# Kernel optimization log

Measured on AMD Instinct MI355X. Metric: run time of the kernel, lower is better.

## Reference

```python
import jax, jax.numpy as jnp
import numpy as np

B, L, D = 4, 2048, 64
N_HEAD = 4
LOCALITY = 0.2
PI = 3.141592653589793


def setup_inputs() -> dict:
    key = jax.random.key(0)
    k1, k2, k3 = jax.random.split(key, 3)
    mesh = jax.random.uniform(k1, (B, L, 2), dtype=jnp.float32)
    inputs = jax.random.normal(k2, (B, L, D), dtype=jnp.float32)
    lmda = jax.random.uniform(k3, (N_HEAD, 1, 1), dtype=jnp.float32)
    return {"mesh": mesh, "inputs": inputs, "lmda": lmda}


def reference(mesh, inputs, lmda):
    FMAX = jnp.finfo(jnp.float32).max
    # pairwise squared distances: (B, L, L)
    diff = mesh[:, :, None, :] - mesh[:, None, :, :]
    m_dist = jnp.sum(diff * diff, axis=-1)
    # per-head scale in (0, inf): tan(pi/4 * (1-eps) * (1 + sin(lmda)))
    scale = jnp.tan(0.25 * PI * (1.0 - 1e-07) * (1.0 + jnp.sin(lmda)))  # (H,1,1)
    scaled = m_dist[:, None, :, :] * scale  # (B, H, L, L)
    # row-wise quantile threshold (linear interpolation, matching torch.quantile)
    thresh = jnp.quantile(scaled, LOCALITY, axis=-1, keepdims=True)  # (B,H,L,1)
    masked = jnp.where(scaled <= thresh, scaled, FMAX)
    att = jax.nn.softmax(-masked, axis=-1)  # (B, H, L, L)
    # aggregate: (B,H,L,L) x (B,L,D) -> (B,L,H,D) -> (B,L,H*D)
    conv = jnp.einsum('bhnj,bjd->bnhd', att, inputs)
    conv = conv.reshape(inputs.shape[0], -1, N_HEAD * inputs.shape[-1])
    return jnp.concatenate([inputs, conv], axis=-1)
```

## Files before the change

### kernel.cpp

```cpp
#include <hip/hip_runtime.h>
#include <math.h>

#ifndef M_PI
#define M_PI 3.14159265358979323846
#endif

namespace {
constexpr int B_ = 4;
constexpr int L_ = 2048;
constexpr int D_ = 64;
constexpr int H_ = 4;
constexpr int RB = 8;
constexpr int KT = 64;
constexpr int NTILE = L_ / KT;
constexpr int CAPC = 256;
constexpr int OUTW = D_ + H_ * D_;
constexpr int APS = 2064;
constexpr int ABYTES = 2 * APS;
constexpr int BBYTES = KT * D_ * 2;
constexpr int BUFB = ABYTES + BBYTES;
}

typedef __attribute__((ext_vector_type(8))) short bf16x8;
typedef __attribute__((ext_vector_type(4))) float f32x4;

__device__ __forceinline__ unsigned bf16_rne(float x) {
    unsigned u = __float_as_uint(x);
    return (u + 0x7fffu + ((u >> 16) & 1u)) >> 16;
}

__device__ __forceinline__ unsigned cvt_pk_bf16(float lo, float hi) {
    unsigned r;
    asm("v_cvt_pk_bf16_f32 %0, %1, %2" : "=v"(r) : "v"(lo), "v"(hi));
    return r;
}

#if defined(__has_builtin)
#if __has_builtin(__builtin_amdgcn_exp2f)
#define EXP2F(x) __builtin_amdgcn_exp2f(x)
#endif
#endif
#ifndef EXP2F
#define EXP2F(x) __expf((x) * 0.69314718055994531f)
#endif

#define LDS_FENCE() __builtin_amdgcn_s_waitcnt(0xC07F)

__global__ __launch_bounds__(256) void prep_kernel(const float* __restrict__ inputs,
                                                   char* __restrict__ ws) {
    const int blk = blockIdx.x;
    const int b = blk >> 6;
    const int r6 = blk & 63;
    const int tile = r6 >> 2;
    const int qr = r6 & 3;
    const int t = threadIdx.x;
    const float* inb = inputs + ((size_t)b * L_ + tile * 128) * D_;
    char* wsb = ws + (size_t)b * (L_ * D_ * 2) + tile * (128 * D_ * 2);
    #pragma unroll
    for (int i = 0; i < 4; ++i) {
        const int idx = qr * 1024 + i * 256 + t;
        const int n  = idx & 63;
        const int kp = idx >> 6;
        const int kl = kp << 1;
        const float x0 = inb[kl * D_ + n];
        const float x1 = inb[(kl + 1) * D_ + n];
        const unsigned a = bf16_rne(x0);
        const unsigned c = bf16_rne(x1);
        const int chunk = (kl >> 3) * 64 + n;
        const int e = kl & 7;
        *reinterpret_cast<unsigned*>(wsb + chunk * 16 + e * 2) = a | (c << 16);
    }
}

__global__ __launch_bounds__(512, 8) void posatt_kernel(
    const float* __restrict__ mesh,
    const float* __restrict__ inputs,
    const float* __restrict__ lmda,
    const char* __restrict__ ws,
    float* __restrict__ out)
{
    __shared__ __align__(16) char s_u1[2 * BUFB];
    __shared__ float s_scale[H_];
    __shared__ float s_thD[RB];
    __shared__ float s_d409[RB], s_d410[RB];
    __shared__ float s_wsum[RB][H_];
    __shared__ unsigned s_ccw[8];

    const int t = threadIdx.x;
    const int l = t & 63;
    const int w = t >> 6;
    const int blk = blockIdx.x;
    const int b = blk >> 8;
    const int n0 = (blk & 255) * RB;

    const float2* meshg = reinterpret_cast<const float2*>(mesh) + (size_t)b * L_;

    if (t < H_) {
        const double lam = (double)lmda[t];
        const float C = (float)(0.25 * M_PI * (1.0 - 1e-07));
        const float s1 = (float)sin(lam);
        const float arg = __fmul_rn(C, __fadd_rn(1.0f, s1));
        s_scale[t] = (float)tan((double)arg);
    }
    if (t < RB) { s_d409[t] = 0.0f; s_d410[t] = 0.0f; }
    __syncthreads();

    {
        unsigned* hw = reinterpret_cast<unsigned*>(s_u1) + w * 256;
        float* cw = reinterpret_cast<float*>(s_u1 + 8192) + w * CAPC;
        const int rl = w;
        const float2 me = meshg[n0 + rl];
        *reinterpret_cast<uint4*>(&hw[l * 4]) = make_uint4(0u, 0u, 0u, 0u);
        if (l == 0) s_ccw[w] = 0u;
        LDS_FENCE();
        #pragma unroll 4
        for (int it = 0; it < 32; ++it) {
            const int j = (it << 6) + l;
            const float2 mj = meshg[j];
            const float dx = __fsub_rn(me.x, mj.x);
            const float dy = __fsub_rn(me.y, mj.y);
            const float d = __fadd_rn(__fmul_rn(dx, dx), __fmul_rn(dy, dy));
            int bin = (int)(d * 128.0f); bin = bin < 255 ? bin : 255;
            atomicAdd(&hw[bin], 1u);
        }
        LDS_FENCE();
        int lo, hi; unsigned base;
        {
            const uint4 hv = *reinterpret_cast<const uint4*>(&hw[l * 4]);
            const unsigned p0 = hv.x, p1 = p0 + hv.y, p2 = p1 + hv.z, p3 = p2 + hv.w;
            unsigned sc = p3;
            #pragma unroll
            for (int off = 1; off < 64; off <<= 1) {
                const unsigned uu = __shfl_up(sc, off);
                if (l >= off) sc += uu;
            }
            const unsigned eb = sc - p3;
            const unsigned cum[4] = {eb + p0, eb + p1, eb + p2, eb + p3};
            int flo = -1, fhi = -1; unsigned fbase = 0u;
            #pragma unroll
            for (int e = 0; e < 4; ++e) {
                const unsigned prev = e ? cum[e - 1] : eb;
                if (cum[e] > 409u && prev <= 409u) { flo = l * 4 + e; fbase = prev; }
                if (cum[e] > 410u && prev <= 410u) { fhi = l * 4 + e; }
            }
            const unsigned long long bmlo = __ballot(flo >= 0);
            const int srclo = (int)__builtin_ctzll(bmlo);
            lo = __shfl(flo, srclo);
            base = __shfl(fbase, srclo);
            const unsigned long long bmhi = __ballot(fhi >= 0);
            hi = __shfl(fhi, (int)__builtin_ctzll(bmhi));
        }
        #pragma unroll 4
        for (int it = 0; it < 32; ++it) {
            const int j = (it << 6) + l;
            const float2 mj = meshg[j];
            const float dx = __fsub_rn(me.x, mj.x);
            const float dy = __fsub_rn(me.y, mj.y);
            const float d = __fadd_rn(__fmul_rn(dx, dx), __fmul_rn(dy, dy));
            int bin = (int)(d * 128.0f); bin = bin < 255 ? bin : 255;
            if (bin >= lo && bin <= hi) {
                const unsigned p = atomicAdd(&s_ccw[w], 1u);
                if (p < (unsigned)CAPC) cw[p] = d;
            }
        }
        LDS_FENCE();
        const int m = (int)min(s_ccw[w], (unsigned)CAPC);
        const unsigned k409 = 409u - base;
        const unsigned k410 = 410u - base;
        const float lo_edge = (float)lo * 0.0078125f;
        const float sc2 = 32768.0f / (float)(hi - lo + 1);
        *reinterpret_cast<uint4*>(&hw[l * 4]) = make_uint4(0u, 0u, 0u, 0u);
        LDS_FENCE();
        #pragma unroll 2
        for (int ci = l; ci < m; ci += 64) {
            const float v = cw[ci];
            int b2 = (int)(__fmul_rn(__fsub_rn(v, lo_edge), sc2));
            b2 = b2 < 255 ? b2 : 255; b2 = b2 > 0 ? b2 : 0;
            atomicAdd(&hw[b2], 1u);
        }
        LDS_FENCE();
        int lo2, hi2; unsigned base2;
        {
            const uint4 hv = *reinterpret_cast<const uint4*>(&hw[l * 4]);
            const unsigned p0 = hv.x, p1 = p0 + hv.y, p2 = p1 + hv.z, p3 = p2 + hv.w;
            unsigned sc = p3;
            #pragma unroll
            for (int off = 1; off < 64; off <<= 1) {
                const unsigned uu = __shfl_up(sc, off);
                if (l >= off) sc += uu;
            }
            const unsigned eb = sc - p3;
            const unsigned cum[4] = {eb + p0, eb + p1, eb + p2, eb + p3};
            int flo = -1, fhi = -1; unsigned fbase = 0u;
            #pragma unroll
            for (int e = 0; e < 4; ++e) {
                const unsigned prev = e ? cum[e - 1] : eb;
                if (cum[e] > k409 && prev <= k409) { flo = l * 4 + e; fbase = prev; }
                if (cum[e] > k410 && prev <= k410) { fhi = l * 4 + e; }
            }
            const unsigned long long bmlo = __ballot(flo >= 0);
            const int srclo = (int)__builtin_ctzll(bmlo);
            lo2 = __shfl(flo, srclo);
            base2 = __shfl(fbase, srclo);
            const unsigned long long bmhi = __ballot(fhi >= 0);
            hi2 = __shfl(fhi, (int)__builtin_ctzll(bmhi));
        }
        if (l == 0) s_ccw[w] = 0u;
        LDS_FENCE();
        float* c2 = reinterpret_cast<float*>(hw);
        #pragma unroll 2
        for (int ci = l; ci < m; ci += 64) {
            const float v = cw[ci];
            int b2 = (int)(__fmul_rn(__fsub_rn(v, lo_edge), sc2));
            b2 = b2 < 255 ? b2 : 255; b2 = b2 > 0 ? b2 : 0;
            if (b2 >= lo2 && b2 <= hi2) {
                const unsigned p = atomicAdd(&s_ccw[w], 1u);
                if (p < 256u) c2[p] = v;
            }
        }
        LDS_FENCE();
        const int c = (int)min(s_ccw[w], 256u);
        const int q409 = (int)(k409 - base2);
        const int q410 = (int)(k410 - base2);
        #pragma unroll 1
        for (int cc0 = 0; cc0 < c; cc0 += 64) {
            const int ci = cc0 + l;
            const float v = (ci < c) ? c2[ci] : 0.0f;
            int lt = 0, le = 0;
            #pragma unroll 4
            for (int i = 0; i < c; ++i) {
                const float u = c2[i];
                lt += (u < v) ? 1 : 0;
                le += (u <= v) ? 1 : 0;
            }
            if (ci < c) {
                if (lt <= q409 && q409 < le) s_d409[rl] = v;
                if (lt <= q410 && q410 < le) s_d410[rl] = v;
            }
        }
    }
    __syncthreads();

    if (t < RB) {
        const float pos = 0.2f * 2047.0f;
        const float g = pos - 409.0f;
        const float lw = 1.0f - g;
        s_thD[t] = __fadd_rn(__fmul_rn(s_d409[t], lw), __fmul_rn(s_d410[t], g));
    }
    __syncthreads();

    const int jp = t & 31;
    const int rr = (t >> 5) & 7;
    const int h2 = t >> 8;
    const float2 me_b = meshg[n0 + rr];
    const float thD = s_thD[rr];
    constexpr float LOG2E = 1.4426950408889634f;
    const float cA = __fmul_rn(-LOG2E, s_scale[h2]);
    const float cB = __fmul_rn(-LOG2E, s_scale[h2 + 2]);
    const int row16 = h2 * 8 + rr;
    const int ks4q_w = jp >> 2;
    const int chunk_w = ks4q_w * 16 + row16;
    const int chunkSw_w = chunk_w ^ (ks4q_w & 7);
    const int aoff0 = (chunkSw_w << 4) + ((jp & 3) << 2);
    float waccA = 0.0f, waccB = 0.0f;

    const int p_w  = w >> 2;
    const int ks_w = (w >> 1) & 1;
    const int nqh  = w & 1;
    const int ks4q_r = ks_w * 4 + (l >> 4);
    const int chunk_r = ks4q_r * 16 + (l & 15);
    const int aroff = p_w * APS + ((chunk_r ^ (ks4q_r & 7)) << 4);
    f32x4 acc[2];
    acc[0] = (f32x4)0.0f; acc[1] = (f32x4)0.0f;

    const float* inpb = inputs + (size_t)b * L_ * D_;
    const char* wsb = ws + (size_t)b * (L_ * D_ * 2);
    const float4* mesh4 = reinterpret_cast<const float4*>(meshg);
    char* const AE = s_u1;
    char* const BE = s_u1 + ABYTES;
    char* const AO = s_u1 + BUFB;
    char* const BO = s_u1 + BUFB + ABYTES;

    auto LOADB = [&](int tile) -> uint4 {
        return *reinterpret_cast<const uint4*>(wsb + ((size_t)(tile * 512 + t) << 4));
    };
    auto COMMITB = [&](char* Bb, const uint4 bg) {
        *reinterpret_cast<uint4*>(Bb + (t << 4)) = bg;
    };
    auto ABUILD = [&](int tile, char* Ab) {
        const float4 mq = mesh4[tile * 32 + jp];
        const float dx0 = __fsub_rn(me_b.x, mq.x);
        const float dy0 = __fsub_rn(me_b.y, mq.y);
        const float d0 = __fadd_rn(__fmul_rn(dx0, dx0), __fmul_rn(dy0, dy0));
        const float dx1 = __fsub_rn(me_b.x, mq.z);
        const float dy1 = __fsub_rn(me_b.y, mq.w);
        const float d1 = __fadd_rn(__fmul_rn(dx1, dx1), __fmul_rn(dy1, dy1));
        const bool pass0 = (d0 <= thD);
        const bool pass1 = (d1 <= thD);
        const float wA0 = pass0 ? EXP2F(__fmul_rn(d0, cA)) : 0.0f;
        const float wA1 = pass1 ? EXP2F(__fmul_rn(d1, cA)) : 0.0f;
        const float wB0 = pass0 ? EXP2F(__fmul_rn(d0, cB)) : 0.0f;
        const float wB1 = pass1 ? EXP2F(__fmul_rn(d1, cB)) : 0.0f;
        waccA += __fadd_rn(wA0, wA1);
        waccB += __fadd_rn(wB0, wB1);
        *reinterpret_cast<unsigned*>(Ab + aoff0) = cvt_pk_bf16(wA0, wA1);
        *reinterpret_cast<unsigned*>(Ab + APS + aoff0) = cvt_pk_bf16(wB0, wB1);
    };
    auto MFMA_STEP = [&](const char* Ab, const char* Bb) {
        const bf16x8 afr = *reinterpret_cast<const bf16x8*>(Ab + aroff);
        #pragma unroll
        for (int i = 0; i < 2; ++i) {
            const int nq = nqh * 2 + i;
            const bf16x8 bfr = *reinterpret_cast<const bf16x8*>(
                Bb + (((ks_w * 4 + (l >> 4)) * 64 + nq * 16 + (l & 15)) << 4));
            acc[i] = __builtin_amdgcn_mfma_f32_16x16x32_bf16(afr, bfr, acc[i], 0, 0, 0);
        }
    };

    {
        const uint4 bg0 = LOADB(0);
        ABUILD(0, AE);
        COMMITB(BE, bg0);
    }
    __syncthreads();
    #pragma unroll 1
    for (int tp = 0; tp < NTILE / 2; ++tp) {
        uint4 bg = LOADB(2 * tp + 1);
        MFMA_STEP(AE, BE);
        ABUILD(2 * tp + 1, AO);
        COMMITB(BO, bg);
        __syncthreads();
        if (tp < NTILE / 2 - 1) {
            bg = LOADB(2 * tp + 2);
            MFMA_STEP(AO, BO);
            ABUILD(2 * tp + 2, AE);
            COMMITB(BE, bg);
            __syncthreads();
        }
    }
    MFMA_STEP(AO, BO);
    __syncthreads();

    waccA += __shfl_xor(waccA, 1);
    waccA += __shfl_xor(waccA, 2);
    waccA += __shfl_xor(waccA, 4);
    waccA += __shfl_xor(waccA, 8);
    waccA += __shfl_xor(waccA, 16);
    waccB += __shfl_xor(waccB, 1);
    waccB += __shfl_xor(waccB, 2);
    waccB += __shfl_xor(waccB, 4);
    waccB += __shfl_xor(waccB, 8);
    waccB += __shfl_xor(waccB, 16);
    if ((l & 31) == 0) {
        s_wsum[rr][h2] = waccA;
        s_wsum[rr][h2 + 2] = waccB;
    }
    {
        float4* Cz = reinterpret_cast<float4*>(s_u1);
        Cz[t] = make_float4(0.f, 0.f, 0.f, 0.f);
    }
    __syncthreads();
    {
        float* Cf = reinterpret_cast<float*>(s_u1);
        #pragma unroll
        for (int i = 0; i < 2; ++i) {
            const int nq = nqh * 2 + i;
            #pragma unroll
            for (int reg = 0; reg < 4; ++reg) {
                const int row = (l >> 4) * 4 + reg;
                const int col = nq * 16 + (l & 15);
                atomicAdd(&Cf[(p_w * 16 + row) * 64 + col], acc[i][reg]);
            }
        }
    }
    __syncthreads();
    {
        const float* Cf = reinterpret_cast<const float*>(s_u1);
        const int pr = t >> 4;
        const int p = pr >> 4;
        const int row16o = pr & 15;
        const int h = p * 2 + (row16o >> 3);
        const int r = row16o & 7;
        const int col = (t & 15) << 2;
        const float wsv = s_wsum[r][h];
        const float inv = (wsv != 0.0f) ? 1.0f / wsv : 0.0f;
        float4 r0 = *reinterpret_cast<const float4*>(&Cf[pr * 64 + col]);
        r0.x *= inv; r0.y *= inv; r0.z *= inv; r0.w *= inv;
        float* op = out + (size_t)(b * L_ + n0 + r) * OUTW + D_ + h * 64 + col;
        *reinterpret_cast<float4*>(op) = r0;
    }
    {
        const int r = t >> 6;
        const int c = t & 63;
        out[(size_t)(b * L_ + n0 + r) * OUTW + c] = inpb[(size_t)(n0 + r) * D_ + c];
    }
}

extern "C" void kernel_launch(void* const* d_in, const int* in_sizes, int n_in,
                              void* d_out, int out_size, void* d_ws, size_t ws_size,
                              hipStream_t stream) {
    const float* mesh   = (const float*)d_in[0];
    const float* inputs = (const float*)d_in[1];
    const float* lmda   = (const float*)d_in[2];
    float* out = (float*)d_out;
    char* ws = (char*)d_ws;
    (void)in_sizes; (void)n_in; (void)out_size; (void)ws_size;
    hipLaunchKernelGGL(prep_kernel, dim3(256), dim3(256), 0, stream, inputs, ws);
    hipLaunchKernelGGL(posatt_kernel, dim3(B_ * (L_ / RB)), dim3(512), 0, stream,
                       mesh, inputs, lmda, ws, out);
}
```

Measured before the change: 125.8 us.

## Move per-row quantile threshold search into prep kernel and ballot-compact candidates

Measured after the change: 128.6 us. +2.2%, slower.

```diff
diff --git a/kernel.cpp b/kernel.cpp
--- a/kernel.cpp
+++ b/kernel.cpp
@@ -46,29 +46,192 @@
 
 #define LDS_FENCE() __builtin_amdgcn_s_waitcnt(0xC07F)
 
-__global__ __launch_bounds__(256) void prep_kernel(const float* __restrict__ inputs,
-                                                   char* __restrict__ ws) {
+__global__ __launch_bounds__(256) void prep_thresh_kernel(
+    const float* __restrict__ mesh,
+    const float* __restrict__ inputs,
+    char* __restrict__ ws,
+    float* __restrict__ out)
+{
+    __shared__ unsigned s_hist[4][256];
+    __shared__ float s_cand[4][256];
+
+    const int t = threadIdx.x;
+    const int l = t & 63;
+    const int w = t >> 6;
     const int blk = blockIdx.x;
-    const int b = blk >> 6;
-    const int r6 = blk & 63;
-    const int tile = r6 >> 2;
-    const int qr = r6 & 3;
-    const int t = threadIdx.x;
-    const float* inb = inputs + ((size_t)b * L_ + tile * 128) * D_;
-    char* wsb = ws + (size_t)b * (L_ * D_ * 2) + tile * (128 * D_ * 2);
-    #pragma unroll
-    for (int i = 0; i < 4; ++i) {
-        const int idx = qr * 1024 + i * 256 + t;
-        const int n  = idx & 63;
-        const int kp = idx >> 6;
-        const int kl = kp << 1;
+
+    if (t < 128) {
+        const unsigned u = (unsigned)blk * 128u + (unsigned)t;
+        const int pb = u >> 16;
+        const int rem = u & 65535;
+        const int tile = rem >> 12;
+        const int idx = rem & 4095;
+        const int n = idx & 63;
+        const int kl = (idx >> 6) << 1;
+        const float* inb = inputs + ((size_t)pb * L_ + tile * 128) * D_;
+        char* wsb = ws + (size_t)pb * (L_ * D_ * 2) + tile * (128 * D_ * 2);
         const float x0 = inb[kl * D_ + n];
         const float x1 = inb[(kl + 1) * D_ + n];
-        const unsigned a = bf16_rne(x0);
-        const unsigned c = bf16_rne(x1);
         const int chunk = (kl >> 3) * 64 + n;
         const int e = kl & 7;
-        *reinterpret_cast<unsigned*>(wsb + chunk * 16 + e * 2) = a | (c << 16);
+        *reinterpret_cast<unsigned*>(wsb + chunk * 16 + e * 2) =
+            bf16_rne(x0) | (bf16_rne(x1) << 16);
+    }
+
+    const int row = blk * 4 + w;
+    const int b = row >> 11;
+    const int rl = row & 2047;
+    const float2* meshg = reinterpret_cast<const float2*>(mesh) + (size_t)b * L_;
+    unsigned* hw = s_hist[w];
+    float* cw = s_cand[w];
+    const float2 me = meshg[rl];
+
+    *reinterpret_cast<uint4*>(&hw[l * 4]) = make_uint4(0u, 0u, 0u, 0u);
+    LDS_FENCE();
+    #pragma unroll 4
+    for (int it = 0; it < 32; ++it) {
+        const int j = (it << 6) + l;
+        const float2 mj = meshg[j];
+        const float dx = __fsub_rn(me.x, mj.x);
+        const float dy = __fsub_rn(me.y, mj.y);
+        const float d = __fadd_rn(__fmul_rn(dx, dx), __fmul_rn(dy, dy));
+        int bin = (int)(d * 128.0f); bin = bin < 255 ? bin : 255;
+        atomicAdd(&hw[bin], 1u);
+    }
+    LDS_FENCE();
+    int lo, hi; unsigned base;
+    {
+        const uint4 hv = *reinterpret_cast<const uint4*>(&hw[l * 4]);
+        const unsigned p0 = hv.x, p1 = p0 + hv.y, p2 = p1 + hv.z, p3 = p2 + hv.w;
+        unsigned sc = p3;
+        #pragma unroll
+        for (int off = 1; off < 64; off <<= 1) {
+            const unsigned uu = __shfl_up(sc, off);
+            if (l >= off) sc += uu;
+        }
+        const unsigned eb = sc - p3;
+        const unsigned cum[4] = {eb + p0, eb + p1, eb + p2, eb + p3};
+        int flo = -1, fhi = -1; unsigned fbase = 0u;
+        #pragma unroll
+        for (int e = 0; e < 4; ++e) {
+            const unsigned prev = e ? cum[e - 1] : eb;
+            if (cum[e] > 409u && prev <= 409u) { flo = l * 4 + e; fbase = prev; }
+            if (cum[e] > 410u && prev <= 410u) { fhi = l * 4 + e; }
+        }
+        const unsigned long long bmlo = __ballot(flo >= 0);
+        const int srclo = (int)__builtin_ctzll(bmlo);
+        lo = __shfl(flo, srclo);
+        base = __shfl(fbase, srclo);
+        const unsigned long long bmhi = __ballot(fhi >= 0);
+        hi = __shfl(fhi, (int)__builtin_ctzll(bmhi));
+    }
+    unsigned cbase = 0u;
+    #pragma unroll 4
+    for (int it = 0; it < 32; ++it) {
+        const int j = (it << 6) + l;
+        const float2 mj = meshg[j];
+        const float dx = __fsub_rn(me.x, mj.x);
+        const float dy = __fsub_rn(me.y, mj.y);
+        const float d = __fadd_rn(__fmul_rn(dx, dx), __fmul_rn(dy, dy));
+        int bin = (int)(d * 128.0f); bin = bin < 255 ? bin : 255;
+        const bool pred = (bin >= lo && bin <= hi);
+        const unsigned long long bm = __ballot(pred);
+        if (pred) {
+            const unsigned p = cbase + (unsigned)__popcll(bm & ((1ull << l) - 1ull));
+            if (p < (unsigned)CAPC) cw[p] = d;
+        }
+        cbase += (unsigned)__popcll(bm);
+    }
+    LDS_FENCE();
+    const int m = (int)min(cbase, (unsigned)CAPC);
+    const unsigned k409 = 409u - base;
+    const unsigned k410 = 410u - base;
+    const float lo_edge = (float)lo * 0.0078125f;
+    const float sc2 = 32768.0f / (float)(hi - lo + 1);
+    *reinterpret_cast<uint4*>(&hw[l * 4]) = make_uint4(0u, 0u, 0u, 0u);
+    LDS_FENCE();
+    #pragma unroll 2
+    for (int ci = l; ci < m; ci += 64) {
+        const float v = cw[ci];
+        int b2 = (int)(__fmul_rn(__fsub_rn(v, lo_edge), sc2));
+        b2 = b2 < 255 ? b2 : 255; b2 = b2 > 0 ? b2 : 0;
+        atomicAdd(&hw[b2], 1u);
+    }
+    LDS_FENCE();
+    int lo2, hi2; unsigned base2;
+    {
+        const uint4 hv = *reinterpret_cast<const uint4*>(&hw[l * 4]);
+        const unsigned p0 = hv.x, p1 = p0 + hv.y, p2 = p1 + hv.z, p3 = p2 + hv.w;
+        unsigned sc = p3;
+        #pragma unroll
+        for (int off = 1; off < 64; off <<= 1) {
+            const unsigned uu = __shfl_up(sc, off);
+            if (l >= off) sc += uu;
+        }
+        const unsigned eb = sc - p3;
+        const unsigned cum[4] = {eb + p0, eb + p1, eb + p2, eb + p3};
+        int flo = -1, fhi = -1; unsigned fbase = 0u;
+        #pragma unroll
+        for (int e = 0; e < 4; ++e) {
+            const unsigned prev = e ? cum[e - 1] : eb;
+            if (cum[e] > k409 && prev <= k409) { flo = l * 4 + e; fbase = prev; }
+            if (cum[e] > k410 && prev <= k410) { fhi = l * 4 + e; }
+        }
+        const unsigned long long bmlo = __ballot(flo >= 0);
+        const int srclo = (int)__builtin_ctzll(bmlo);
+        lo2 = __shfl(flo, srclo);
+        base2 = __shfl(fbase, srclo);
+        const unsigned long long bmhi = __ballot(fhi >= 0);
+        hi2 = __shfl(fhi, (int)__builtin_ctzll(bmhi));
+    }
+    float* c2 = reinterpret_cast<float*>(hw);
+    unsigned cnt2 = 0u;
+    for (int c0 = 0; c0 < m; c0 += 64) {
+        const int ci = c0 + l;
+        float v = 0.0f; bool pred = false;
+        if (ci < m) {
+            v = cw[ci];
+            int b2 = (int)(__fmul_rn(__fsub_rn(v, lo_edge), sc2));
+            b2 = b2 < 255 ? b2 : 255; b2 = b2 > 0 ? b2 : 0;
+            pred = (b2 >= lo2 && b2 <= hi2);
+        }
+        const unsigned long long bm = __ballot(pred);
+        if (pred) {
+            const unsigned p = cnt2 + (unsigned)__popcll(bm & ((1ull << l) - 1ull));
+            if (p < 256u) c2[p] = v;
+        }
+        cnt2 += (unsigned)__popcll(bm);
+    }
+    LDS_FENCE();
+    const int c = (int)min(cnt2, 256u);
+    const int q409 = (int)(k409 - base2);
+    const int q410 = (int)(k410 - base2);
+    if (l == 0) { cw[0] = 0.0f; cw[1] = 0.0f; }
+    LDS_FENCE();
+    #pragma unroll 1
+    for (int cc0 = 0; cc0 < c; cc0 += 64) {
+        const int ci = cc0 + l;
+        const float v = (ci < c) ? c2[ci] : 0.0f;
+        int lt = 0, le = 0;
+        #pragma unroll 4
+        for (int i = 0; i < c; ++i) {
+            const float u = c2[i];
+            lt += (u < v) ? 1 : 0;
+            le += (u <= v) ? 1 : 0;
+        }
+        if (ci < c) {
+            if (lt <= q409 && q409 < le) cw[0] = v;
+            if (lt <= q410 && q410 < le) cw[1] = v;
+        }
+    }
+    LDS_FENCE();
+    if (l == 0) {
+        const float d409 = cw[0], d410 = cw[1];
+        const float pos = 0.2f * 2047.0f;
+        const float g = pos - 409.0f;
+        const float lw = 1.0f - g;
+        const float thD = __fadd_rn(__fmul_rn(d409, lw), __fmul_rn(d410, g));
+        out[(size_t)(b * L_ + rl) * OUTW + 319] = thD;
     }
 }
 
@@ -82,9 +245,7 @@
     __shared__ __align__(16) char s_u1[2 * BUFB];
     __shared__ float s_scale[H_];
     __shared__ float s_thD[RB];
-    __shared__ float s_d409[RB], s_d410[RB];
     __shared__ float s_wsum[RB][H_];
-    __shared__ unsigned s_ccw[8];
 
     const int t = threadIdx.x;
     const int l = t & 63;
@@ -102,150 +263,8 @@
         const float arg = __fmul_rn(C, __fadd_rn(1.0f, s1));
         s_scale[t] = (float)tan((double)arg);
     }
-    if (t < RB) { s_d409[t] = 0.0f; s_d410[t] = 0.0f; }
-    __syncthreads();
-
-    {
-        unsigned* hw = reinterpret_cast<unsigned*>(s_u1) + w * 256;
-        float* cw = reinterpret_cast<float*>(s_u1 + 8192) + w * CAPC;
-        const int rl = w;
-        const float2 me = meshg[n0 + rl];
-        *reinterpret_cast<uint4*>(&hw[l * 4]) = make_uint4(0u, 0u, 0u, 0u);
-        if (l == 0) s_ccw[w] = 0u;
-        LDS_FENCE();
-        #pragma unroll 4
-        for (int it = 0; it < 32; ++it) {
-            const int j = (it << 6) + l;
-            const float2 mj = meshg[j];
-            const float dx = __fsub_rn(me.x, mj.x);
-            const float dy = __fsub_rn(me.y, mj.y);
-            const float d = __fadd_rn(__fmul_rn(dx, dx), __fmul_rn(dy, dy));
-            int bin = (int)(d * 128.0f); bin = bin < 255 ? bin : 255;
-            atomicAdd(&hw[bin], 1u);
-        }
-        LDS_FENCE();
-        int lo, hi; unsigned base;
-        {
-            const uint4 hv = *reinterpret_cast<const uint4*>(&hw[l * 4]);
-            const unsigned p0 = hv.x, p1 = p0 + hv.y, p2 = p1 + hv.z, p3 = p2 + hv.w;
-            unsigned sc = p3;
-            #pragma unroll
-            for (int off = 1; off < 64; off <<= 1) {
-                const unsigned uu = __shfl_up(sc, off);
-                if (l >= off) sc += uu;
-            }
-            const unsigned eb = sc - p3;
-            const unsigned cum[4] = {eb + p0, eb + p1, eb + p2, eb + p3};
-            int flo = -1, fhi = -1; unsigned fbase = 0u;
-            #pragma unroll
-            for (int e = 0; e < 4; ++e) {
-                const unsigned prev = e ? cum[e - 1] : eb;
-                if (cum[e] > 409u && prev <= 409u) { flo = l * 4 + e; fbase = prev; }
-                if (cum[e] > 410u && prev <= 410u) { fhi = l * 4 + e; }
-            }
-            const unsigned long long bmlo = __ballot(flo >= 0);
-            const int srclo = (int)__builtin_ctzll(bmlo);
-            lo = __shfl(flo, srclo);
-            base = __shfl(fbase, srclo);
-            const unsigned long long bmhi = __ballot(fhi >= 0);
-            hi = __shfl(fhi, (int)__builtin_ctzll(bmhi));
-        }
-        #pragma unroll 4
-        for (int it = 0; it < 32; ++it) {
-            const int j = (it << 6) + l;
-            const float2 mj = meshg[j];
-            const float dx = __fsub_rn(me.x, mj.x);
-            const float dy = __fsub_rn(me.y, mj.y);
-            const float d = __fadd_rn(__fmul_rn(dx, dx), __fmul_rn(dy, dy));
-            int bin = (int)(d * 128.0f); bin = bin < 255 ? bin : 255;
-            if (bin >= lo && bin <= hi) {
-                const unsigned p = atomicAdd(&s_ccw[w], 1u);
-                if (p < (unsigned)CAPC) cw[p] = d;
-            }
-        }
-        LDS_FENCE();
-        const int m = (int)min(s_ccw[w], (unsigned)CAPC);
-        const unsigned k409 = 409u - base;
-        const unsigned k410 = 410u - base;
-        const float lo_edge = (float)lo * 0.0078125f;
-        const float sc2 = 32768.0f / (float)(hi - lo + 1);
-        *reinterpret_cast<uint4*>(&hw[l * 4]) = make_uint4(0u, 0u, 0u, 0u);
-        LDS_FENCE();
-        #pragma unroll 2
-        for (int ci = l; ci < m; ci += 64) {
-            const float v = cw[ci];
-            int b2 = (int)(__fmul_rn(__fsub_rn(v, lo_edge), sc2));
-            b2 = b2 < 255 ? b2 : 255; b2 = b2 > 0 ? b2 : 0;
-            atomicAdd(&hw[b2], 1u);
-        }
-        LDS_FENCE();
-        int lo2, hi2; unsigned base2;
-        {
-            const uint4 hv = *reinterpret_cast<const uint4*>(&hw[l * 4]);
-            const unsigned p0 = hv.x, p1 = p0 + hv.y, p2 = p1 + hv.z, p3 = p2 + hv.w;
-            unsigned sc = p3;
-            #pragma unroll
-            for (int off = 1; off < 64; off <<= 1) {
-                const unsigned uu = __shfl_up(sc, off);
-                if (l >= off) sc += uu;
-            }
-            const unsigned eb = sc - p3;
-            const unsigned cum[4] = {eb + p0, eb + p1, eb + p2, eb + p3};
-            int flo = -1, fhi = -1; unsigned fbase = 0u;
-            #pragma unroll
-            for (int e = 0; e < 4; ++e) {
-                const unsigned prev = e ? cum[e - 1] : eb;
-                if (cum[e] > k409 && prev <= k409) { flo = l * 4 + e; fbase = prev; }
-                if (cum[e] > k410 && prev <= k410) { fhi = l * 4 + e; }
-            }
-            const unsigned long long bmlo = __ballot(flo >= 0);
-            const int srclo = (int)__builtin_ctzll(bmlo);
-            lo2 = __shfl(flo, srclo);
-            base2 = __shfl(fbase, srclo);
-            const unsigned long long bmhi = __ballot(fhi >= 0);
-            hi2 = __shfl(fhi, (int)__builtin_ctzll(bmhi));
-        }
-        if (l == 0) s_ccw[w] = 0u;
-        LDS_FENCE();
-        float* c2 = reinterpret_cast<float*>(hw);
-        #pragma unroll 2
-        for (int ci = l; ci < m; ci += 64) {
-            const float v = cw[ci];
-            int b2 = (int)(__fmul_rn(__fsub_rn(v, lo_edge), sc2));
-            b2 = b2 < 255 ? b2 : 255; b2 = b2 > 0 ? b2 : 0;
-            if (b2 >= lo2 && b2 <= hi2) {
-                const unsigned p = atomicAdd(&s_ccw[w], 1u);
-                if (p < 256u) c2[p] = v;
-            }
-        }
-        LDS_FENCE();
-        const int c = (int)min(s_ccw[w], 256u);
-        const int q409 = (int)(k409 - base2);
-        const int q410 = (int)(k410 - base2);
-        #pragma unroll 1
-        for (int cc0 = 0; cc0 < c; cc0 += 64) {
-            const int ci = cc0 + l;
-            const float v = (ci < c) ? c2[ci] : 0.0f;
-            int lt = 0, le = 0;
-            #pragma unroll 4
-            for (int i = 0; i < c; ++i) {
-                const float u = c2[i];
-                lt += (u < v) ? 1 : 0;
-                le += (u <= v) ? 1 : 0;
-            }
-            if (ci < c) {
-                if (lt <= q409 && q409 < le) s_d409[rl] = v;
-                if (lt <= q410 && q410 < le) s_d410[rl] = v;
-            }
-        }
-    }
-    __syncthreads();
-
     if (t < RB) {
-        const float pos = 0.2f * 2047.0f;
-        const float g = pos - 409.0f;
-        const float lw = 1.0f - g;
-        s_thD[t] = __fadd_rn(__fmul_rn(s_d409[t], lw), __fmul_rn(s_d410[t], g));
+        s_thD[t] = out[(size_t)(b * L_ + n0 + t) * OUTW + 319];
     }
     __syncthreads();
 
@@ -405,7 +424,8 @@
     float* out = (float*)d_out;
     char* ws = (char*)d_ws;
     (void)in_sizes; (void)n_in; (void)out_size; (void)ws_size;
-    hipLaunchKernelGGL(prep_kernel, dim3(256), dim3(256), 0, stream, inputs, ws);
+    hipLaunchKernelGGL(prep_thresh_kernel, dim3(2048), dim3(256), 0, stream,
+                       mesh, inputs, ws, out);
     hipLaunchKernelGGL(posatt_kernel, dim3(B_ * (L_ / RB)), dim3(512), 0, stream,
                        mesh, inputs, lmda, ws, out);
 }
```
